# Kernel tuning notes

Hardware: AMD Instinct MI355X
Metric: run time of the kernel (lower is better)

Reference implementation:

```python
import jax, jax.numpy as jnp
import numpy as np

G = 32            # group_dim
N = 2             # feature batch (becomes 3N after repeat)
H = 192
W = 192
C_EXTRA = 32      # channels of the extra input tensor
POOLING_SIZE = (5, 9, 17)
POOLING_CHAN = (1, 1, 1)  # scaled by group_dim inside the module


def conv1x1(x, w, b):
    # x: [B, Cin, H, W], w: [Cout, Cin], b: [Cout]
    return jnp.einsum('bchw,oc->bohw', x, w) + b[None, :, None, None]


def integral_image(x):
    # x: [B, C, H, W] -> summed-area table [B, C, H+1, W+1] with zero top row / left col
    s = jnp.cumsum(jnp.cumsum(x, axis=2), axis=3)
    return jnp.pad(s, ((0, 0), (0, 0), (1, 0), (1, 0)))


def box_sums(S, half, h, w):
    # S: [B, C, h+1, w+1]; returns per-pixel box sums [B, C, h, w] and area [h, w]
    y = jnp.arange(h)
    x = jnp.arange(w)
    y0 = jnp.maximum(y - half, 0)
    y1 = jnp.minimum(y + 1 + half, h)
    x0 = jnp.maximum(x - half, 0)
    x1 = jnp.minimum(x + 1 + half, w)
    Sy0 = S[:, :, y0, :]
    Sy1 = S[:, :, y1, :]
    s = Sy1[:, :, :, x1] - Sy1[:, :, :, x0] - Sy0[:, :, :, x1] + Sy0[:, :, :, x0]
    area = ((y1 - y0)[:, None] * (x1 - x0)[None, :]).astype(S.dtype)
    return s, area


def setup_inputs() -> dict:
    key = jax.random.key(0)
    ks = jax.random.split(key, 10)
    C = G + C_EXTRA  # channels after concat with image_ctx
    c1_out = (G + 2) // 2 * 4
    inp = {
        'feature': jax.random.normal(ks[0], (N, G, H, W), jnp.float32),
        'extra': jax.random.normal(ks[1], (3 * N, C_EXTRA, H, W), jnp.float32),
        'w_ctx': jax.random.normal(ks[2], (G, G), jnp.float32) * 0.05,
        'b_ctx': jnp.zeros((G,), jnp.float32),
        'w1': jax.random.normal(ks[3], (c1_out, C), jnp.float32) * 0.05,
        'b1': jnp.zeros((c1_out,), jnp.float32),
    }
    for i in range(3):
        oc = 2 * G * POOLING_CHAN[i]
        inp['w_s%d' % i] = jax.random.normal(ks[4 + i], (oc, 2 * C), jnp.float32) * 0.05
        inp['b_s%d' % i] = jnp.zeros((oc,), jnp.float32)
    return inp


def reference(feature, extra, w_ctx, b_ctx, w1, b1,
              w_s0, b_s0, w_s1, b_s1, w_s2, b_s2):
    img_ctx = conv1x1(feature, w_ctx, b_ctx)          # [N, G, H, W]
    img_ctx = jnp.repeat(img_ctx, 3, axis=0)          # [3N, G, H, W]
    x = jnp.concatenate([img_ctx, extra], axis=1)     # [3N, C, H, W]
    _, _, h, w = x.shape

    outs = [conv1x1(x, w1, b1)]

    S1 = integral_image(x)
    S2 = integral_image(x * x)

    scale_params = ((w_s0, b_s0), (w_s1, b_s1), (w_s2, b_s2))
    for ps, (ws, bs) in zip(POOLING_SIZE, scale_params):
        half = ps // 2
        s1, area = box_sums(S1, half, h, w)
        s2, _ = box_sums(S2, half, h, w)
        mean = s1 / area
        var = s2 / area - mean * mean
        outs.append(conv1x1(jnp.concatenate([mean, var], axis=1), ws, bs))

    return jnp.concatenate(outs, axis=1)  # [3N, 68 + 3*64 = 260, H, W]
```

## Files before the change

### kernel.cpp

```cpp
#include <hip/hip_runtime.h>

#define H 192
#define W 192
#define HW (H*W)
#define G 32
#define C 64
#define C2 128
#define C1 68
#define B 6
#define NB 2
#define OUTC 260
#define STRIP 48
#define STRIP_R 48


__global__ __launch_bounds__(256) void ctx_kernel(
    const float* __restrict__ feature, const float* __restrict__ w_ctx,
    const float* __restrict__ b_ctx, float* __restrict__ ctx)
{
    int p = blockIdx.x * 256 + threadIdx.x;
    int b = blockIdx.y;
    float f[G];
    const float* fp = feature + (size_t)b * G * HW + p;
#pragma unroll
    for (int k = 0; k < G; k++) f[k] = fp[k * HW];
    float* op = ctx + (size_t)b * G * HW + p;
    for (int o = 0; o < G; o++) {
        float acc = b_ctx[o];
#pragma unroll
        for (int k = 0; k < G; k++) acc += w_ctx[o * G + k] * f[k];
        op[o * HW] = acc;
    }
}

__global__ __launch_bounds__(256) void conv1_kernel(
    const float* __restrict__ ctx, const float* __restrict__ extra,
    const float* __restrict__ w1, const float* __restrict__ b1,
    float* __restrict__ out)
{
    int p = blockIdx.x * 256 + threadIdx.x;
    int b = blockIdx.y;
    float xv[C];
    const float* cp = ctx + (size_t)(b / 3) * G * HW + p;
#pragma unroll
    for (int k = 0; k < G; k++) xv[k] = cp[k * HW];
    const float* ep = extra + (size_t)b * G * HW + p;
#pragma unroll
    for (int k = 0; k < G; k++) xv[G + k] = ep[k * HW];
    float* op = out + (size_t)b * OUTC * HW + p;
    for (int o = 0; o < C1; o++) {
        float acc = b1[o];
#pragma unroll
        for (int k = 0; k < C; k++) acc += w1[o * C + k] * xv[k];
        op[o * HW] = acc;
    }
}


template<int CTRL, int RM>
__device__ __forceinline__ float dpp_mov0(float x) {
    return __int_as_float(__builtin_amdgcn_update_dpp(
        0, __float_as_int(x), CTRL, RM, 0xf, false));
}
__device__ __forceinline__ float wave_iscan(float x) {
    x += dpp_mov0<0x111, 0xf>(x);
    x += dpp_mov0<0x112, 0xf>(x);
    x += dpp_mov0<0x114, 0xf>(x);
    x += dpp_mov0<0x118, 0xf>(x);
    x += dpp_mov0<0x142, 0xa>(x);
    x += dpp_mov0<0x143, 0xc>(x);
    return x;
}

__global__ __launch_bounds__(256) void transpose_wi_kernel(
    const float* __restrict__ w0, const float* __restrict__ w1,
    const float* __restrict__ w2, float* __restrict__ wTi)
{
    int i = blockIdx.x * 256 + threadIdx.x;
    if (i >= 3 * C * C2) return;
    int si = i / (C * C2);
    int r = i % (C * C2);
    const float* ws = (si == 0) ? w0 : (si == 1) ? w1 : w2;
    int o = r / C2, ci = r % C2;
    int dst = (ci < C) ? (ci * (2 * C) + o) : ((ci - C) * (2 * C) + C + o);
    wTi[si * (C2 * C) + dst] = ws[r];
}

__global__ __launch_bounds__(192) void mv_all_kernel(
    const float* __restrict__ ctx, const float* __restrict__ extra,
    int bbase, int nbs, float* __restrict__ mv)
{
    __shared__ float2 pls[2][3][W];
    __shared__ float2 wsum[2][3][3];
    const int hk0 = 2, hk1 = 4, hk2 = 8;
    const int hks[3] = {hk0, hk1, hk2};

    int w = threadIdx.x;
    int lane = w & 63;
    int wv = w >> 6;
    int c = blockIdx.x;
    int bz = blockIdx.z;
    int b = bbase + bz;
    const float* src = (c < G) ? (ctx + ((size_t)(b / 3) * G + c) * HW)
                               : (extra + ((size_t)b * G + (c - G)) * HW);
    int h0 = blockIdx.y * STRIP_R;

    float s1[3] = {0.f, 0.f, 0.f}, s2[3] = {0.f, 0.f, 0.f};
#pragma unroll
    for (int dy = -hk2; dy <= hk2; ++dy) {
        int y = h0 + dy;
        float v = (y >= 0 && y < H) ? src[y * W + w] : 0.f;
        float vv = v * v;
        if (dy >= -hk0 && dy <= hk0) { s1[0] += v; s2[0] += vv; }
        if (dy >= -hk1 && dy <= hk1) { s1[1] += v; s2[1] += vv; }
        s1[2] += v; s2[2] += vv;
    }

    float inv_nc[3];
    int x1i[3], x0m[3];
#pragma unroll
    for (int k = 0; k < 3; ++k) {
        int x0 = max(w - hks[k], 0), x1 = min(w + hks[k], W - 1);
        x1i[k] = x1;
        x0m[k] = w - hks[k] - 1;
        inv_nc[k] = 1.0f / (float)(x1 - x0 + 1);
    }
    size_t sstride = (size_t)nbs * C * HW;
    float2* mvp = (float2*)mv + ((size_t)bz * C + c) * HW;

    for (int h = h0; h < h0 + STRIP_R; ++h) {
        if (h > h0) {
#pragma unroll
            for (int k = 0; k < 3; ++k) {
                int ya = h + hks[k], ys = h - hks[k] - 1;
                if (ya < H)  { float v = src[ya * W + w]; s1[k] += v; s2[k] = fmaf(v, v, s2[k]); }
                if (ys >= 0) { float v = src[ys * W + w]; s1[k] -= v; s2[k] = fmaf(-v, v, s2[k]); }
            }
        }
        int buf = h & 1;
        float p1[3], p2[3];
#pragma unroll
        for (int k = 0; k < 3; ++k) { p1[k] = wave_iscan(s1[k]); p2[k] = wave_iscan(s2[k]); }
        if (lane == 63) {
#pragma unroll
            for (int k = 0; k < 3; ++k) wsum[buf][k][wv] = make_float2(p1[k], p2[k]);
        }
        __syncthreads();
#pragma unroll
        for (int k = 0; k < 3; ++k) {
            float2 w0v = wsum[buf][k][0];
            float2 w1v = wsum[buf][k][1];
            float o1 = 0.f, o2 = 0.f;
            if (wv >= 1) { o1 += w0v.x; o2 += w0v.y; }
            if (wv >= 2) { o1 += w1v.x; o2 += w1v.y; }
            pls[buf][k][w] = make_float2(p1[k] + o1, p2[k] + o2);
        }
        __syncthreads();
#pragma unroll
        for (int k = 0; k < 3; ++k) {
            float2 hi = pls[buf][k][x1i[k]];
            int xm = x0m[k];
            float2 lo = pls[buf][k][xm < 0 ? 0 : xm];
            if (xm < 0) { lo.x = 0.f; lo.y = 0.f; }
            float t1 = hi.x - lo.x;
            float t2 = hi.y - lo.y;
            float inv_nr;
            if (h >= hks[k] && h + hks[k] < H) inv_nr = 1.0f / (float)(2 * hks[k] + 1);
            else inv_nr = 1.0f / (float)(min(h + hks[k], H - 1) - max(h - hks[k], 0) + 1);
            float ia = inv_nr * inv_nc[k];
            float mean = t1 * ia;
            float var = fmaf(t2, ia, -(mean * mean));
            mvp[(size_t)k * sstride + h * W + w] = make_float2(mean, var);
        }
    }
}

__global__ __launch_bounds__(256) void sconv_all_kernel(
    const float* __restrict__ mv, const float* __restrict__ wTi,
    const float* __restrict__ bs0, const float* __restrict__ bs1,
    const float* __restrict__ bs2,
    int bbase, int nbs, float* __restrict__ out)
{
    int p = blockIdx.x * 256 + threadIdx.x;
    int bz = blockIdx.y;
    int si = blockIdx.z;
    size_t sstride = (size_t)nbs * C * HW;
    const float2* xp = (const float2*)mv + (size_t)si * sstride + (size_t)bz * C * HW + p;
    const float* wp = wTi + si * (C2 * C);
    float acc[C];
#pragma unroll
    for (int o = 0; o < C; ++o) acc[o] = 0.f;
#pragma unroll 2
    for (int c = 0; c < C; ++c) {
        float2 v = xp[(size_t)c * HW];
        const float* wrow = wp + c * (2 * C);
#pragma unroll
        for (int o = 0; o < C; ++o)
            acc[o] = fmaf(wrow[o], v.x, fmaf(wrow[C + o], v.y, acc[o]));
    }
    const float* bs = (si == 0) ? bs0 : (si == 1) ? bs1 : bs2;
    float* op = out + ((size_t)(bbase + bz) * OUTC + C1 + si * C) * HW + p;
#pragma unroll
    for (int o = 0; o < C; ++o) op[o * HW] = acc[o] + bs[o];
}


__global__ __launch_bounds__(256) void transpose_w_kernel(
    const float* __restrict__ wsrc, float* __restrict__ wT, int oc, int ic)
{
    int i = blockIdx.x * 256 + threadIdx.x;
    if (i >= oc * ic) return;
    int o = i / ic, c = i % ic;
    wT[c * oc + o] = wsrc[i];
}

__global__ __launch_bounds__(192) void mv_kernel(
    const float* __restrict__ ctx, const float* __restrict__ extra,
    int half, int bbase, float* __restrict__ mv)
{
    __shared__ float ls1[2][W];
    __shared__ float ls2[2][W];
    int w = threadIdx.x;
    int c = blockIdx.x;
    int s = blockIdx.y;
    int bz = blockIdx.z;
    int b = bbase + bz;
    const float* src = (c < G)
        ? (ctx + ((size_t)(b / 3) * G + c) * HW)
        : (extra + ((size_t)b * G + (c - G)) * HW);

    int h0 = s * STRIP;
    int ya = max(h0 - half, 0);
    int yb = min(h0 + half, H - 1);
    float s1 = 0.f, s2 = 0.f;
    for (int y = ya; y <= yb; y++) { float v = src[y * W + w]; s1 += v; s2 += v * v; }

    int x0 = max(w - half, 0);
    int x1 = min(w + half, W - 1);
    float ncols = (float)(x1 - x0 + 1);

    size_t obase = ((size_t)bz * C2 + c) * HW;

    for (int h = h0; h < h0 + STRIP; h++) {
        if (h > h0) {
            int yadd = h + half;
            int ysub = h - half - 1;
            if (yadd <= H - 1) { float v = src[yadd * W + w]; s1 += v; s2 += v * v; }
            if (ysub >= 0)     { float v = src[ysub * W + w]; s1 -= v; s2 -= v * v; }
        }
        int buf = h & 1;
        ls1[buf][w] = s1;
        ls2[buf][w] = s2;
        __syncthreads();
        float t1 = 0.f, t2 = 0.f;
        for (int x = x0; x <= x1; x++) { t1 += ls1[buf][x]; t2 += ls2[buf][x]; }
        int nrows = min(h + half, H - 1) - max(h - half, 0) + 1;
        float inv_area = 1.0f / ((float)nrows * ncols);
        float mean = t1 * inv_area;
        float var  = t2 * inv_area - mean * mean;
        mv[obase + h * W + w] = mean;
        mv[obase + (size_t)C * HW + h * W + w] = var;
    }
}

__global__ __launch_bounds__(256) void sconv_kernel(
    const float* __restrict__ mv, const float* __restrict__ wT,
    const float* __restrict__ bsc, int bbase, int co, float* __restrict__ out)
{
    int p = blockIdx.x * 256 + threadIdx.x;
    int bz = blockIdx.y;
    int b = bbase + bz;
    const float* xp = mv + (size_t)bz * C2 * HW + p;
    float acc[C];
#pragma unroll
    for (int o = 0; o < C; o++) acc[o] = 0.f;
#pragma unroll 2
    for (int c = 0; c < C2; c++) {
        float v = xp[(size_t)c * HW];
        const float* wrow = wT + c * C;
#pragma unroll
        for (int o = 0; o < C; o++) acc[o] += wrow[o] * v;
    }
    float* op = out + ((size_t)b * OUTC + co) * HW + p;
#pragma unroll
    for (int o = 0; o < C; o++) op[o * HW] = acc[o] + bsc[o];
}


extern "C" void kernel_launch(void* const* d_in, const int* in_sizes, int n_in,
                              void* d_out, int out_size, void* d_ws, size_t ws_size,
                              hipStream_t stream) {
    const float* feature = (const float*)d_in[0];
    const float* extra   = (const float*)d_in[1];
    const float* w_ctx   = (const float*)d_in[2];
    const float* b_ctx   = (const float*)d_in[3];
    const float* w1      = (const float*)d_in[4];
    const float* b1      = (const float*)d_in[5];
    const float* w_s[3]  = {(const float*)d_in[6], (const float*)d_in[8], (const float*)d_in[10]};
    const float* b_s[3]  = {(const float*)d_in[7], (const float*)d_in[9], (const float*)d_in[11]};
    float* out = (float*)d_out;

    float* ctx = (float*)d_ws;
    float* wT  = ctx + (size_t)NB * G * HW;
    float* mv  = wT + 3 * C2 * C;

    size_t base_bytes = ((size_t)NB * G * HW + 3 * C2 * C) * 4;
    size_t mv_new = (size_t)B * 3 * C * HW * 2 * 4;
    size_t mv_full = (size_t)B * C2 * HW * 4;
    bool newpath = ws_size >= base_bytes + mv_new;

    ctx_kernel<<<dim3(HW / 256, NB), 256, 0, stream>>>(feature, w_ctx, b_ctx, ctx);
    conv1_kernel<<<dim3(HW / 256, B), 256, 0, stream>>>(ctx, extra, w1, b1, out);

    if (newpath) {
        transpose_wi_kernel<<<dim3((3 * C * C2 + 255) / 256), 256, 0, stream>>>(
            w_s[0], w_s[1], w_s[2], wT);
        mv_all_kernel<<<dim3(C, H / STRIP_R, B), W, 0, stream>>>(ctx, extra, 0, B, mv);
        sconv_all_kernel<<<dim3(HW / 256, B, 3), 256, 0, stream>>>(
            mv, wT, b_s[0], b_s[1], b_s[2], 0, B, out);
    } else {
        for (int si = 0; si < 3; si++) {
            transpose_w_kernel<<<dim3((C2 * C + 255) / 256), 256, 0, stream>>>(
                w_s[si], wT + si * C2 * C, C, C2);
        }
        const int halves[3] = {2, 4, 8};
        bool batched = ws_size >= base_bytes + mv_full;
        if (batched) {
            for (int si = 0; si < 3; si++) {
                mv_kernel<<<dim3(C, H / STRIP, B), W, 0, stream>>>(ctx, extra, halves[si], 0, mv);
                sconv_kernel<<<dim3(HW / 256, B), 256, 0, stream>>>(
                    mv, wT + si * C2 * C, b_s[si], 0, C1 + si * C, out);
            }
        } else {
            for (int si = 0; si < 3; si++) {
                for (int b = 0; b < B; b++) {
                    mv_kernel<<<dim3(C, H / STRIP, 1), W, 0, stream>>>(ctx, extra, halves[si], b, mv);
                    sconv_kernel<<<dim3(HW / 256, 1), 256, 0, stream>>>(
                        mv, wT + si * C2 * C, b_s[si], b, C1 + si * C, out);
                }
            }
        }
    }
}
```

Baseline: 705.4 us.

## Tile box-stat kernel into single-wave column strips and split sconv outputs via LDS

The moving-window mean/variance kernel now runs one 64-lane wave per 48-column tile with an 8-column halo. Horizontal box sums come from wave-level scan plus shuffles instead of a 3-wave LDS scan with two block barriers per row. The scale-conv kernel uses 512 threads, each computing 32 of the 64 output channels, and stages input channels through double-buffered shared memory so the two halves share loads. This cuts register pressure and sync overhead, at the cost of recomputing halo columns (64 lanes for 48 outputs) and adding LDS traffic and barriers.

```diff
diff --git a/kernel.cpp b/kernel.cpp
--- a/kernel.cpp
+++ b/kernel.cpp
@@ -11,7 +11,7 @@
 #define NB 2
 #define OUTC 260
 #define STRIP 48
-#define STRIP_R 48
+#define SCH 8
 
 
 __global__ __launch_bounds__(256) void ctx_kernel(
@@ -86,122 +86,148 @@
     wTi[si * (C2 * C) + dst] = ws[r];
 }
 
-__global__ __launch_bounds__(192) void mv_all_kernel(
+__global__ __launch_bounds__(64) void mv_all_kernel2(
     const float* __restrict__ ctx, const float* __restrict__ extra,
     int bbase, int nbs, float* __restrict__ mv)
 {
-    __shared__ float2 pls[2][3][W];
-    __shared__ float2 wsum[2][3][3];
     const int hk0 = 2, hk1 = 4, hk2 = 8;
     const int hks[3] = {hk0, hk1, hk2};
 
-    int w = threadIdx.x;
-    int lane = w & 63;
-    int wv = w >> 6;
+    int lane = threadIdx.x;
     int c = blockIdx.x;
+    int sy = blockIdx.y & 3;
+    int sx = blockIdx.y >> 2;
     int bz = blockIdx.z;
     int b = bbase + bz;
     const float* src = (c < G) ? (ctx + ((size_t)(b / 3) * G + c) * HW)
                                : (extra + ((size_t)b * G + (c - G)) * HW);
-    int h0 = blockIdx.y * STRIP_R;
+    int col = sx * 48 - 8 + lane;
+    bool colok = (col >= 0 && col < W);
+    int h0 = sy * 48;
 
     float s1[3] = {0.f, 0.f, 0.f}, s2[3] = {0.f, 0.f, 0.f};
 #pragma unroll
     for (int dy = -hk2; dy <= hk2; ++dy) {
         int y = h0 + dy;
-        float v = (y >= 0 && y < H) ? src[y * W + w] : 0.f;
+        float v = (colok && y >= 0 && y < H) ? src[y * W + col] : 0.f;
         float vv = v * v;
         if (dy >= -hk0 && dy <= hk0) { s1[0] += v; s2[0] += vv; }
         if (dy >= -hk1 && dy <= hk1) { s1[1] += v; s2[1] += vv; }
         s1[2] += v; s2[2] += vv;
     }
 
+    bool outok = (lane >= 8 && lane < 56);
     float inv_nc[3];
-    int x1i[3], x0m[3];
 #pragma unroll
     for (int k = 0; k < 3; ++k) {
-        int x0 = max(w - hks[k], 0), x1 = min(w + hks[k], W - 1);
-        x1i[k] = x1;
-        x0m[k] = w - hks[k] - 1;
+        int x0 = max(col - hks[k], 0), x1 = min(col + hks[k], W - 1);
         inv_nc[k] = 1.0f / (float)(x1 - x0 + 1);
     }
     size_t sstride = (size_t)nbs * C * HW;
     float2* mvp = (float2*)mv + ((size_t)bz * C + c) * HW;
 
-    for (int h = h0; h < h0 + STRIP_R; ++h) {
+    for (int h = h0; h < h0 + 48; ++h) {
         if (h > h0) {
 #pragma unroll
             for (int k = 0; k < 3; ++k) {
                 int ya = h + hks[k], ys = h - hks[k] - 1;
-                if (ya < H)  { float v = src[ya * W + w]; s1[k] += v; s2[k] = fmaf(v, v, s2[k]); }
-                if (ys >= 0) { float v = src[ys * W + w]; s1[k] -= v; s2[k] = fmaf(-v, v, s2[k]); }
-            }
-        }
-        int buf = h & 1;
-        float p1[3], p2[3];
-#pragma unroll
-        for (int k = 0; k < 3; ++k) { p1[k] = wave_iscan(s1[k]); p2[k] = wave_iscan(s2[k]); }
-        if (lane == 63) {
-#pragma unroll
-            for (int k = 0; k < 3; ++k) wsum[buf][k][wv] = make_float2(p1[k], p2[k]);
-        }
-        __syncthreads();
+                if (colok) {
+                    if (ya < H)  { float v = src[ya * W + col]; s1[k] += v; s2[k] = fmaf(v, v, s2[k]); }
+                    if (ys >= 0) { float v = src[ys * W + col]; s1[k] -= v; s2[k] = fmaf(-v, v, s2[k]); }
+                }
+            }
+        }
 #pragma unroll
         for (int k = 0; k < 3; ++k) {
-            float2 w0v = wsum[buf][k][0];
-            float2 w1v = wsum[buf][k][1];
-            float o1 = 0.f, o2 = 0.f;
-            if (wv >= 1) { o1 += w0v.x; o2 += w0v.y; }
-            if (wv >= 2) { o1 += w1v.x; o2 += w1v.y; }
-            pls[buf][k][w] = make_float2(p1[k] + o1, p2[k] + o2);
-        }
-        __syncthreads();
-#pragma unroll
-        for (int k = 0; k < 3; ++k) {
-            float2 hi = pls[buf][k][x1i[k]];
-            int xm = x0m[k];
-            float2 lo = pls[buf][k][xm < 0 ? 0 : xm];
-            if (xm < 0) { lo.x = 0.f; lo.y = 0.f; }
-            float t1 = hi.x - lo.x;
-            float t2 = hi.y - lo.y;
-            float inv_nr;
-            if (h >= hks[k] && h + hks[k] < H) inv_nr = 1.0f / (float)(2 * hks[k] + 1);
-            else inv_nr = 1.0f / (float)(min(h + hks[k], H - 1) - max(h - hks[k], 0) + 1);
-            float ia = inv_nr * inv_nc[k];
-            float mean = t1 * ia;
-            float var = fmaf(t2, ia, -(mean * mean));
-            mvp[(size_t)k * sstride + h * W + w] = make_float2(mean, var);
-        }
-    }
-}
-
-__global__ __launch_bounds__(256) void sconv_all_kernel(
+            float p1 = wave_iscan(s1[k]);
+            float p2 = wave_iscan(s2[k]);
+            int ihi = lane + hks[k];
+            int ilo = lane - hks[k] - 1;
+            float h1 = __shfl(p1, ihi & 63);
+            float h2 = __shfl(p2, ihi & 63);
+            float l1 = __shfl(p1, ilo & 63);
+            float l2 = __shfl(p2, ilo & 63);
+            if (ilo < 0) { l1 = 0.f; l2 = 0.f; }
+            if (outok) {
+                float t1 = h1 - l1;
+                float t2 = h2 - l2;
+                float inv_nr;
+                if (h >= hks[k] && h + hks[k] < H) inv_nr = 1.0f / (float)(2 * hks[k] + 1);
+                else inv_nr = 1.0f / (float)(min(h + hks[k], H - 1) - max(h - hks[k], 0) + 1);
+                float ia = inv_nr * inv_nc[k];
+                float mean = t1 * ia;
+                float var = fmaf(t2, ia, -(mean * mean));
+                mvp[(size_t)k * sstride + h * W + col] = make_float2(mean, var);
+            }
+        }
+    }
+}
+
+__global__ __launch_bounds__(512) void sconv_all_kernel2(
     const float* __restrict__ mv, const float* __restrict__ wTi,
     const float* __restrict__ bs0, const float* __restrict__ bs1,
     const float* __restrict__ bs2,
     int bbase, int nbs, float* __restrict__ out)
 {
-    int p = blockIdx.x * 256 + threadIdx.x;
+    __shared__ float2 xs[2][SCH][256];
+    int tid = threadIdx.x;
+    int px = tid & 255;
+    int oh = tid >> 8;
+    int p0 = blockIdx.x * 256;
     int bz = blockIdx.y;
     int si = blockIdx.z;
     size_t sstride = (size_t)nbs * C * HW;
-    const float2* xp = (const float2*)mv + (size_t)si * sstride + (size_t)bz * C * HW + p;
+    const float2* xp = (const float2*)mv + (size_t)si * sstride + (size_t)bz * C * HW + p0;
     const float* wp = wTi + si * (C2 * C);
-    float acc[C];
-#pragma unroll
-    for (int o = 0; o < C; ++o) acc[o] = 0.f;
-#pragma unroll 2
-    for (int c = 0; c < C; ++c) {
-        float2 v = xp[(size_t)c * HW];
-        const float* wrow = wp + c * (2 * C);
-#pragma unroll
-        for (int o = 0; o < C; ++o)
-            acc[o] = fmaf(wrow[o], v.x, fmaf(wrow[C + o], v.y, acc[o]));
-    }
+
+    float2 r[4];
+#pragma unroll
+    for (int i = 0; i < 4; ++i) {
+        int idx = i * 512 + tid;
+        r[i] = xp[(size_t)(idx >> 8) * HW + (idx & 255)];
+    }
+#pragma unroll
+    for (int i = 0; i < 4; ++i) {
+        int idx = i * 512 + tid;
+        xs[0][idx >> 8][idx & 255] = r[i];
+    }
+    __syncthreads();
+
+    float acc[32];
+#pragma unroll
+    for (int o = 0; o < 32; ++o) acc[o] = 0.f;
+
+    for (int cc = 0; cc < C / SCH; ++cc) {
+        int cur = cc & 1;
+        if (cc < C / SCH - 1) {
+#pragma unroll
+            for (int i = 0; i < 4; ++i) {
+                int idx = i * 512 + tid;
+                r[i] = xp[(size_t)((cc + 1) * SCH + (idx >> 8)) * HW + (idx & 255)];
+            }
+        }
+#pragma unroll
+        for (int c = 0; c < SCH; ++c) {
+            float2 v = xs[cur][c][px];
+            const float* wrow = wp + (cc * SCH + c) * (2 * C) + oh * 32;
+#pragma unroll
+            for (int o = 0; o < 32; ++o)
+                acc[o] = fmaf(wrow[o], v.x, fmaf(wrow[C + o], v.y, acc[o]));
+        }
+        if (cc < C / SCH - 1) {
+#pragma unroll
+            for (int i = 0; i < 4; ++i) {
+                int idx = i * 512 + tid;
+                xs[cur ^ 1][idx >> 8][idx & 255] = r[i];
+            }
+            __syncthreads();
+        }
+    }
+
     const float* bs = (si == 0) ? bs0 : (si == 1) ? bs1 : bs2;
-    float* op = out + ((size_t)(bbase + bz) * OUTC + C1 + si * C) * HW + p;
-#pragma unroll
-    for (int o = 0; o < C; ++o) op[o * HW] = acc[o] + bs[o];
+    float* op = out + ((size_t)(bbase + bz) * OUTC + C1 + si * C + oh * 32) * HW + p0 + px;
+#pragma unroll
+    for (int o = 0; o < 32; ++o) op[(size_t)o * HW] = acc[o] + bs[oh * 32 + o];
 }
 
 
@@ -315,8 +341,8 @@
     if (newpath) {
         transpose_wi_kernel<<<dim3((3 * C * C2 + 255) / 256), 256, 0, stream>>>(
             w_s[0], w_s[1], w_s[2], wT);
-        mv_all_kernel<<<dim3(C, H / STRIP_R, B), W, 0, stream>>>(ctx, extra, 0, B, mv);
-        sconv_all_kernel<<<dim3(HW / 256, B, 3), 256, 0, stream>>>(
+        mv_all_kernel2<<<dim3(C, 16, B), 64, 0, stream>>>(ctx, extra, 0, B, mv);
+        sconv_all_kernel2<<<dim3(HW / 256, B, 3), 512, 0, stream>>>(
             mv, wT, b_s[0], b_s[1], b_s[2], 0, B, out);
     } else {
         for (int si = 0; si < 3; si++) {
```

Measured after the change: 1.275 ms. 1.81x slower.
